# Performance work log

Hardware: AMD Instinct MI355X
Metric: run time of the kernel (lower is better)

Reference implementation:

```python
import jax, jax.numpy as jnp
import numpy as np

# dims: B pages, P boxes/page, TOTAL flat boxes, D model, H heads, C coords, Z rel positions, L layers
B, P, TOTAL, D, H, C, Z, L = 16, 512, 6400, 256, 8, 2, 64, 4
HS = D // H          # head size = 32
PAD_COLS = 448       # columns >= PAD_COLS are padding (-1)


def setup_inputs():
    key = jax.random.key(0)
    ks = jax.random.split(key, 10)
    embeds = jax.random.normal(ks[0], (TOTAL, D), jnp.float32)
    page_ids = jax.random.randint(ks[1], (B, P), 0, TOTAL)
    page_ids = page_ids.at[:, PAD_COLS:].set(-1)
    xmin = jax.random.uniform(ks[2], (TOTAL,)) * 0.9
    xmax = xmin + jax.random.uniform(ks[3], (TOTAL,)) * 0.1 + 0.01
    ymin = jax.random.uniform(ks[4], (TOTAL,)) * 0.9
    ymax = ymin + jax.random.uniform(ks[5], (TOTAL,)) * 0.1 + 0.01
    kk = jax.random.split(ks[6], 12)
    w = lambda k, *s: jax.random.normal(k, s, jnp.float32) * 0.02
    return dict(
        embeds=embeds, xmin=xmin, xmax=xmax, ymin=ymin, ymax=ymax,
        width=xmax - xmin, height=ymax - ymin,
        empty_embed=jax.random.normal(ks[7], (D,), jnp.float32),
        position_embedding=jax.random.normal(ks[8], (Z, D), jnp.float32),
        cq_w=w(kk[0], L, D, D), cq_b=jnp.zeros((L, D)),
        ck_w=w(kk[1], L, D, D), ck_b=jnp.zeros((L, D)),
        pk_w=w(kk[2], L, D, D), pk_b=jnp.zeros((L, D)),
        pq_w=w(kk[3], L, D, D), pq_b=jnp.zeros((L, D)),
        cv_w=w(kk[4], L, D, D), cv_b=jnp.zeros((L, D)),
        out_w=w(kk[5], L, D, D), out_b=jnp.zeros((L, D)),
        res1=jnp.full((L,), 0.1, jnp.float32), res2=jnp.full((L,), 0.1, jnp.float32),
        ln1_g=jnp.ones((L, D)), ln1_b=jnp.zeros((L, D)),
        ln2_g=jnp.ones((L, D)), ln2_b=jnp.zeros((L, D)),
        ff1_w=w(kk[6], L, D, 2 * D), ff1_b=jnp.zeros((L, 2 * D)),
        ff2_w=w(kk[7], L, 2 * D, D), ff2_b=jnp.zeros((L, D)),
        page_ids=page_ids,
    )


def _layer_norm(x, g, b, eps=1e-5):
    m = jnp.mean(x, axis=-1, keepdims=True)
    v = jnp.mean((x - m) ** 2, axis=-1, keepdims=True)
    return (x - m) * jax.lax.rsqrt(v + eps) * g + b


def _compute_rel(x0, x1, y0, y1, w, h, n_rel):
    # clamped to +-n_rel//2 and shifted into [0, n_rel)
    cx = (x0 + x1) * 0.5
    cy = (y0 + y1) * 0.5
    dx = jnp.round((cx[:, None, :] - cx[:, :, None]) / jnp.maximum(w[:, :, None], 1e-3))
    dy = jnp.round((cy[:, None, :] - cy[:, :, None]) / jnp.maximum(h[:, :, None], 1e-3))
    half = n_rel // 2
    rel = jnp.stack([dx, dy], axis=-1)
    return (jnp.clip(rel, -half, half - 1) + half).astype(jnp.int32)


def _forward(embeds, xmin, xmax, ymin, ymax, width, height, empty_embed,
             position_embedding, cq_w, cq_b, ck_w, ck_b, pk_w, pk_b, pq_w, pq_b,
             cv_w, cv_b, out_w, out_b, res1, res2, ln1_g, ln1_b, ln2_g, ln2_b,
             ff1_w, ff1_b, ff2_w, ff2_b, page_ids):
    mask = page_ids != -1                                           # [B,P]
    gth = lambda a: a[page_ids]                                     # flat -> [B,P]
    x = jnp.concatenate([jnp.broadcast_to(empty_embed, (B, 1, D)),
                         embeds[page_ids]], axis=1)                 # [B,N,D], N=P+1
    maskc = jnp.concatenate([jnp.ones((B, 1), bool), mask], axis=1) # [B,N]
    rel = _compute_rel(gth(xmin), gth(xmax), gth(ymin), gth(ymax),
                       gth(width), gth(height), Z)                  # [B,P,P,2]
    N = P + 1
    relc = jnp.zeros((B, N, N, 2), jnp.int32).at[:, 1:, 1:, :].set(rel)
    nopos = jnp.ones((B, N, N), bool).at[:, 1:, 1:].set(False)      # disable pos terms on CLS
    scale = 1.0 / float(np.sqrt(HS))
    neg = jnp.finfo(jnp.float32).min

    for l in range(L):
        q = (x @ cq_w[l] + cq_b[l]).reshape(B, N, H, HS)
        k = (x @ ck_w[l] + ck_b[l]).reshape(B, N, H, HS)
        c2c = jnp.einsum('bihd,bjhd->bijh', q, k)                   # [B,N,N,H]
        pk = (position_embedding @ pk_w[l] + pk_b[l]).reshape(Z, C, H, HS // C)
        pq = (position_embedding @ pq_w[l] + pq_b[l]).reshape(Z, C, H, HS // C)
        qc = q.reshape(B, N, H, C, HS // C)
        kc = k.reshape(B, N, H, C, HS // C)
        # c2p: score query against every relative-position key, then gather by index
        c2p = jnp.take_along_axis(jnp.einsum('bihcd,zchd->bizch', qc, pk),
                                  relc[..., None], axis=2)          # [B,N,N,C,H]
        # p2c: score position queries against content keys, gather along position axis
        p2c = jnp.take_along_axis(jnp.einsum('bjhcd,zchd->bzjch', kc, pq),
                                  relc[..., None], axis=1)          # [B,N,N,C,H]
        pos = jnp.sum(c2p + p2c, axis=3) * (~nopos)[..., None].astype(x.dtype)
        logits = (c2c + pos) * scale
        weights = jax.nn.softmax(
            jnp.where(maskc[:, None, :, None], logits, neg), axis=2)
        v = (x @ cv_w[l] + cv_b[l]).reshape(B, N, H, HS)
        upd = jnp.einsum('bijh,bjhd->bihd', weights, v).reshape(B, N, D) @ out_w[l] + out_b[l]
        x = _layer_norm(x + upd * res1[l], ln1_g[l], ln1_b[l])
        ff = jax.nn.gelu(x @ ff1_w[l] + ff1_b[l], approximate=False) @ ff2_w[l] + ff2_b[l]
        x = _layer_norm(x + ff * res2[l], ln2_g[l], ln2_b[l])

    # drop CLS and zero padded boxes (padded static-shape analogue of embeds[:,1:][mask])
    return x[:, 1:] * mask[..., None].astype(x.dtype)


def reference(embeds, xmin, xmax, ymin, ymax, width, height, empty_embed,
              position_embedding, cq_w, cq_b, ck_w, ck_b, pk_w, pk_b, pq_w, pq_b,
              cv_w, cv_b, out_w, out_b, res1, res2, ln1_g, ln1_b, ln2_g, ln2_b,
              ff1_w, ff1_b, ff2_w, ff2_b, page_ids):
    return _forward(embeds, xmin, xmax, ymin, ymax, width, height, empty_embed,
                    position_embedding, cq_w, cq_b, ck_w, ck_b, pk_w, pk_b, pq_w, pq_b,
                    cv_w, cv_b, out_w, out_b, res1, res2, ln1_g, ln1_b, ln2_g, ln2_b,
                    ff1_w, ff1_b, ff2_w, ff2_b, page_ids)
```

## Files before the change

### kernel.cpp

```cpp
#include <hip/hip_runtime.h>
#include <math.h>

#define BB 16
#define PP 512
#define DD 256
#define HH 8
#define NPAD 512
#define NVAL 449
#define MM (BB*PP)
#define NROWS (BB*HH*NPAD)

typedef unsigned short u16;
typedef __bf16 v8bf __attribute__((ext_vector_type(8)));
typedef float v4f __attribute__((ext_vector_type(4)));
typedef unsigned short u16x8 __attribute__((ext_vector_type(8)));
typedef unsigned short u16x4 __attribute__((ext_vector_type(4)));

static __device__ __forceinline__ float b2f(u16 u) {
  unsigned v = ((unsigned)u) << 16;
  return __builtin_bit_cast(float, v);
}
static __device__ __forceinline__ u16 f2b(float f) {
  unsigned x = __builtin_bit_cast(unsigned, f);
  unsigned lsb = (x >> 16) & 1u;
  x += 0x7fffu + lsb;
  return (u16)(x >> 16);
}
static __device__ __forceinline__ v8bf ldg8(const u16* p) {
  u16x8 u = *(const u16x8*)p;
  return __builtin_bit_cast(v8bf, u);
}
static __device__ __forceinline__ void gload16(const u16* g, u16* l) {
  __builtin_amdgcn_global_load_lds(
      (__attribute__((address_space(1))) void*)(g),
      (__attribute__((address_space(3))) void*)(l), 16, 0, 0);
}

__global__ void k_prep(const float* embeds, const float* xmin, const float* xmax,
                       const float* ymin, const float* ymax, const float* width,
                       const float* height, const float* empty_embed, const int* page_ids,
                       float* xf, u16* xb, float* gcx, float* gcy, float* gw, float* gh_) {
  int bx = blockIdx.x;
  int b = bx >> 9, r = bx & 511;
  int t = threadIdx.x;
  int c0 = t * 4;
  const float* src = nullptr;
  if (r == 0) src = empty_embed;
  else if (r <= 448) {
    int gi = page_ids[b * PP + (r - 1)];
    src = embeds + (size_t)gi * DD;
  }
  float4 fv = make_float4(0.f, 0.f, 0.f, 0.f);
  if (src) fv = *(const float4*)(src + c0);
  size_t row = (size_t)b * NPAD + r;
  *(float4*)(xf + row * DD + c0) = fv;
  u16x4 bv; bv[0] = f2b(fv.x); bv[1] = f2b(fv.y); bv[2] = f2b(fv.z); bv[3] = f2b(fv.w);
  *(u16x4*)(xb + row * DD + c0) = bv;
  if (t == 0) {
    int p = r;
    int gi = page_ids[b * PP + p];
    float cx = 0.f, cy = 0.f, ww = 1.f, hh = 1.f;
    if (gi >= 0) {
      cx = 0.5f * (xmin[gi] + xmax[gi]);
      cy = 0.5f * (ymin[gi] + ymax[gi]);
      ww = fmaxf(width[gi], 1e-3f);
      hh = fmaxf(height[gi], 1e-3f);
    }
    gcx[b * PP + p] = cx; gcy[b * PP + p] = cy;
    gw[b * PP + p] = ww;  gh_[b * PP + p] = hh;
  }
}

__global__ __launch_bounds__(64) void k_rel(const float* gcx, const float* gcy,
                                            const float* gw, const float* gh_, u16* relp) {
  int bx = blockIdx.x;
  int b = bx >> 9, i = bx & 511;
  int t = threadIdx.x;
  float cxi = 0.f, cyi = 0.f, wi = 1.f, hi = 1.f;
  if (i > 0) {
    cxi = gcx[b * PP + i - 1]; cyi = gcy[b * PP + i - 1];
    wi = gw[b * PP + i - 1];   hi = gh_[b * PP + i - 1];
  }
  u16* dst = relp + ((size_t)b * NPAD + i) * NPAD;
#pragma unroll
  for (int jj = 0; jj < 8; jj++) {
    int j = jj * 64 + t;
    u16 pk = (u16)(32 | (32 << 8));
    if (j > 0) {
      float cxj = gcx[b * PP + j - 1], cyj = gcy[b * PP + j - 1];
      float dxf = rintf((cxj - cxi) / wi);
      float dyf = rintf((cyj - cyi) / hi);
      int zx = (int)(fminf(fmaxf(dxf, -32.f), 31.f)) + 32;
      int zy = (int)(fminf(fmaxf(dyf, -32.f), 31.f)) + 32;
      pk = (u16)(zx | (zy << 8));
    }
    dst[j] = pk;
  }
}

__global__ __launch_bounds__(256) void k_wT(const float* cq, const float* ck, const float* cv,
                                            const float* ow, const float* f1, const float* f2,
                                            u16* wT) {
  __shared__ u16 lds[32][33];
  int bx = blockIdx.x;
  int l = bx >> 9, r = bx & 511;
  const float* src; int N, k0, n0; u16* dst; int dstStride;
  if (r < 192) {
    int mat = r / 64, rr = r % 64;
    k0 = (rr >> 3) * 32; n0 = (rr & 7) * 32;
    src = (mat == 0 ? cq : mat == 1 ? ck : cv) + (size_t)l * 65536;
    N = 256; dst = wT + (size_t)l * 524288 + mat * 65536; dstStride = 256;
  } else if (r < 256) {
    int rr = r - 192;
    k0 = (rr >> 3) * 32; n0 = (rr & 7) * 32;
    src = ow + (size_t)l * 65536; N = 256;
    dst = wT + (size_t)l * 524288 + 196608; dstStride = 256;
  } else if (r < 384) {
    int rr = r - 256;
    k0 = (rr >> 4) * 32; n0 = (rr & 15) * 32;
    src = f1 + (size_t)l * 131072; N = 512;
    dst = wT + (size_t)l * 524288 + 262144; dstStride = 256;
  } else {
    int rr = r - 384;
    k0 = (rr >> 3) * 32; n0 = (rr & 7) * 32;
    src = f2 + (size_t)l * 131072; N = 256;
    dst = wT + (size_t)l * 524288 + 393216; dstStride = 512;
  }
  int tx = threadIdx.x & 31, ty = threadIdx.x >> 5;
#pragma unroll
  for (int yy = 0; yy < 4; yy++) {
    int y = ty + yy * 8;
    lds[y][tx] = f2b(src[(size_t)(k0 + y) * N + n0 + tx]);
  }
  __syncthreads();
#pragma unroll
  for (int yy = 0; yy < 4; yy++) {
    int y = ty + yy * 8;
    dst[(size_t)(n0 + y) * dstStride + k0 + tx] = lds[tx][y];
  }
}

__global__ __launch_bounds__(256) void k_posproj(const float* pe, const float* pkw, const float* pkb,
                                                 const float* pqw, const float* pqb,
                                                 u16* pkfsw, u16* pqfsw) {
  int gid = blockIdx.x * 256 + threadIdx.x;
  int d = gid & 15, z = (gid >> 4) & 63, ch = (gid >> 10) & 15, l = (gid >> 14) & 3, tab = gid >> 16;
  const float* W = (tab ? pqw : pkw) + (size_t)l * 65536;
  const float* Bb = (tab ? pqb : pkb) + (size_t)l * 256;
  int col = (ch >> 3) * 128 + (ch & 7) * 16 + d;
  float s = Bb[col];
  const float* per = pe + (size_t)z * 256;
  for (int kk = 0; kk < 256; kk++) s += per[kk] * W[(size_t)kk * 256 + col];
  u16* dst = tab ? pqfsw : pkfsw;
  dst[(((size_t)l * 16 + ch) * 64 + z) * 16 + d] = f2b(s);
}

template <int EPI>
__global__ __launch_bounds__(256) void k_gemm(const u16* A, const u16* W, int K,
                                              const float* bias0, const float* bias1, const float* bias2,
                                              void* out0, void* out1, void* out2) {
  __shared__ u16 As[2][2048];
  __shared__ u16 Bs[2][2048];
  int w = threadIdx.x >> 6, lane = threadIdx.x & 63;
  int la = lane & 15, lg = lane >> 4;
  int wm = w & 1, wn = w >> 1;
  int m0 = blockIdx.x * 64;
  int n0 = blockIdx.y * 64;
  int arow = w * 16 + (lane >> 2);
  int koff = (lane & 3) * 8;
  const u16* gA = A + (size_t)(m0 + arow) * K + koff;
  const u16* gB = W + (size_t)(n0 + arow) * K + koff;
  v4f acc[2][2] = {};
  int nt = K >> 5;
  gload16(gA, &As[0][w * 512]);
  gload16(gB, &Bs[0][w * 512]);
  __syncthreads();
  for (int t = 0; t < nt; t++) {
    int cur = t & 1;
    if (t + 1 < nt) {
      int k2 = (t + 1) << 5;
      gload16(gA + k2, &As[cur ^ 1][w * 512]);
      gload16(gB + k2, &Bs[cur ^ 1][w * 512]);
    }
    const u16* as = As[cur];
    const u16* bs = Bs[cur];
    v8bf a0 = ldg8(as + (wm * 32 + la) * 32 + lg * 8);
    v8bf a1 = ldg8(as + (wm * 32 + 16 + la) * 32 + lg * 8);
    v8bf b0 = ldg8(bs + (wn * 32 + la) * 32 + lg * 8);
    v8bf b1 = ldg8(bs + (wn * 32 + 16 + la) * 32 + lg * 8);
    acc[0][0] = __builtin_amdgcn_mfma_f32_16x16x32_bf16(a0, b0, acc[0][0], 0, 0, 0);
    acc[0][1] = __builtin_amdgcn_mfma_f32_16x16x32_bf16(a0, b1, acc[0][1], 0, 0, 0);
    acc[1][0] = __builtin_amdgcn_mfma_f32_16x16x32_bf16(a1, b0, acc[1][0], 0, 0, 0);
    acc[1][1] = __builtin_amdgcn_mfma_f32_16x16x32_bf16(a1, b1, acc[1][1], 0, 0, 0);
    __syncthreads();
  }
#pragma unroll
  for (int fi = 0; fi < 2; fi++)
#pragma unroll
    for (int fj = 0; fj < 2; fj++)
#pragma unroll
      for (int rr = 0; rr < 4; rr++) {
        int m = m0 + wm * 32 + fi * 16 + lg * 4 + rr;
        int n = n0 + wn * 32 + fj * 16 + la;
        float v = acc[fi][fj][rr];
        if (EPI == 0) {
          const float* bp = (n < 256 ? bias0 : n < 512 ? bias1 : bias2);
          v += bp[n & 255];
          int b = m >> 9, i = m & 511, h = (n & 255) >> 5, d = n & 31;
          if (n < 512) {
            u16* dst = (u16*)(n < 256 ? out0 : out1);
            dst[(((size_t)(b * 8 + h)) * NPAD + i) * 32 + d] = f2b(v);
          } else {
            ((u16*)out2)[(((size_t)(b * 8 + h)) * 32 + d) * NPAD + i] = f2b(v);
          }
        } else if (EPI == 1) {
          ((u16*)out0)[(size_t)m * 256 + n] = f2b(v + bias0[n]);
        } else {
          float x = v + bias0[n];
          float g = 0.5f * x * (1.0f + erff(x * 0.70710678118654752f));
          ((u16*)out0)[(size_t)m * 512 + n] = f2b(g);
        }
      }
}

__global__ __launch_bounds__(256) void k_gemmA(const u16* opartb, const float* lpart,
                                               const u16* W, const float* bias, u16* y16) {
  __shared__ u16 As[2][2048];
  __shared__ u16 Bs[2][2048];
  int w = threadIdx.x >> 6, lane = threadIdx.x & 63;
  int la = lane & 15, lg = lane >> 4;
  int wm = w & 1, wn = w >> 1;
  int m0 = blockIdx.x * 64;
  int n0 = blockIdx.y * 64;
  int arow = w * 16 + (lane >> 2);
  int koff = (lane & 3) * 8;
  int m = m0 + arow, bb = m >> 9, ii = m & 511;
  const u16* gB = W + (size_t)(n0 + arow) * 256 + koff;
  v4f acc[2][2] = {};
  size_t rb0 = ((size_t)(bb * 8)) * NPAD + ii;
#define STAGE_A(hh, buf) do { \
    size_t rbase = rb0 + (size_t)(hh) * NPAD; \
    float l_ = lpart[rbase] + lpart[NROWS + rbase] + lpart[2u*NROWS + rbase] + lpart[3u*NROWS + rbase]; \
    float inv_ = 1.0f / l_; \
    u16x8 a0_ = *(const u16x8*)(opartb + rbase * 32 + koff); \
    u16x8 a1_ = *(const u16x8*)(opartb + ((size_t)NROWS + rbase) * 32 + koff); \
    u16x8 a2_ = *(const u16x8*)(opartb + ((size_t)2u * NROWS + rbase) * 32 + koff); \
    u16x8 a3_ = *(const u16x8*)(opartb + ((size_t)3u * NROWS + rbase) * 32 + koff); \
    u16x8 r_; \
    _Pragma("unroll") \
    for (int e = 0; e < 8; e++) \
      r_[e] = f2b((b2f(a0_[e]) + b2f(a1_[e]) + b2f(a2_[e]) + b2f(a3_[e])) * inv_); \
    *(u16x8*)(&As[buf][arow * 32 + koff]) = r_; \
  } while (0)
  STAGE_A(0, 0);
  gload16(gB, &Bs[0][w * 512]);
  __syncthreads();
  for (int t = 0; t < 8; t++) {
    int cur = t & 1;
    if (t + 1 < 8) {
      STAGE_A(t + 1, cur ^ 1);
      gload16(gB + ((t + 1) << 5), &Bs[cur ^ 1][w * 512]);
    }
    const u16* as = As[cur];
    const u16* bs = Bs[cur];
    v8bf a0 = ldg8(as + (wm * 32 + la) * 32 + lg * 8);
    v8bf a1 = ldg8(as + (wm * 32 + 16 + la) * 32 + lg * 8);
    v8bf b0 = ldg8(bs + (wn * 32 + la) * 32 + lg * 8);
    v8bf b1 = ldg8(bs + (wn * 32 + 16 + la) * 32 + lg * 8);
    acc[0][0] = __builtin_amdgcn_mfma_f32_16x16x32_bf16(a0, b0, acc[0][0], 0, 0, 0);
    acc[0][1] = __builtin_amdgcn_mfma_f32_16x16x32_bf16(a0, b1, acc[0][1], 0, 0, 0);
    acc[1][0] = __builtin_amdgcn_mfma_f32_16x16x32_bf16(a1, b0, acc[1][0], 0, 0, 0);
    acc[1][1] = __builtin_amdgcn_mfma_f32_16x16x32_bf16(a1, b1, acc[1][1], 0, 0, 0);
    __syncthreads();
  }
#undef STAGE_A
#pragma unroll
  for (int fi = 0; fi < 2; fi++)
#pragma unroll
    for (int fj = 0; fj < 2; fj++)
#pragma unroll
      for (int rr = 0; rr < 4; rr++) {
        int mm = m0 + wm * 32 + fi * 16 + lg * 4 + rr;
        int n = n0 + wn * 32 + fj * 16 + la;
        y16[(size_t)mm * 256 + n] = f2b(acc[fi][fj][rr] + bias[n]);
      }
}

__global__ __launch_bounds__(256) void k_tab(const u16* qh, const u16* kh,
                                             const u16* pkfsw, const u16* pqfsw,
                                             u16* tabC2, u16* tabP2, int l) {
  __shared__ __align__(16) u16 qs[4][8][32];
  const u16* srcp = blockIdx.z ? kh : qh;
  const u16* tbl = blockIdx.z ? pqfsw : pkfsw;
  u16* dst = blockIdx.z ? tabP2 : tabC2;
  int b = blockIdx.y, i0 = blockIdx.x * 4;
  int t = threadIdx.x;
  {
    int flat = t * 4;
    int si = flat >> 8, sh = (flat >> 5) & 7, sd = flat & 31;
    *(u16x4*)&qs[si][sh][sd] =
        *(const u16x4*)(srcp + (((size_t)(b * 8 + sh)) * NPAD + i0 + si) * 32 + sd);
  }
  __syncthreads();
  int z = t & 63, cg = t >> 6;
#pragma unroll
  for (int cc = 0; cc < 4; cc++) {
    int ch = cg * 4 + cc, c = ch >> 3, h = ch & 7;
    const u16* pp = tbl + (((size_t)l * 16 + ch) * 64 + z) * 16;
    u16x8 w0 = *(const u16x8*)pp;
    u16x8 w1 = *(const u16x8*)(pp + 8);
#pragma unroll
    for (int ii = 0; ii < 4; ii++) {
      const u16* qq = &qs[ii][h][c * 16];
      float s = 0.f;
#pragma unroll
      for (int d = 0; d < 8; d++) s += b2f(qq[d]) * b2f(w0[d]);
#pragma unroll
      for (int d = 0; d < 8; d++) s += b2f(qq[d + 8]) * b2f(w1[d]);
      dst[(((size_t)b * NPAD + i0 + ii) * 64 + z) * 16 + ch] = f2b(s);
    }
  }
}

__global__ __launch_bounds__(512) void k_attn(const u16* qh, const u16* kh, const u16* vtp,
                                              const u16* tabC2, const u16* tabP2, const u16* relp,
                                              u16* opartb, float* lpart) {
  __shared__ __align__(16) u16 posb[8][16][68];
  __shared__ __align__(16) u16 ps[8][16][72];
  int bid = blockIdx.x;
  int idx = (bid & 7) * 256 + (bid >> 3);
  int b = idx >> 7;
  int rest = idx & 127;
  int i0 = (rest >> 2) * 16;
  int part = rest & 3;
  int t = threadIdx.x, w = t >> 6, lane = t & 63;
  int la = lane & 15, lg = lane >> 4;
  v8bf qa = ldg8(qh + (((size_t)(b * 8 + w)) * NPAD + i0 + la) * 32 + lg * 8);
  float lrow[4] = {0.f, 0.f, 0.f, 0.f};
  v4f o0 = {}; v4f o1 = {};
  const float scale = 0.17677669529663687f;
  const float MC = 8.0f;
  const u16* kbase = kh + ((size_t)(b * 8 + w)) * NPAD * 32;
  const u16* vbase = vtp + ((size_t)(b * 8 + w)) * 32 * NPAD;
  const u16* rbase = relp + ((size_t)b * NPAD + i0) * NPAD;
  int ntile = (part == 3) ? 1 : 2;
  for (int tt = 0; tt < ntile; tt++) {
    int j0 = (part * 2 + tt) * 64;
#pragma unroll
    for (int pp = 0; pp < 2; pp++) {
      int p = t + pp * 512;
      int si = p >> 6, sj = p & 63;
      int ig = i0 + si, jg = j0 + sj;
      float pos[8] = {0.f, 0.f, 0.f, 0.f, 0.f, 0.f, 0.f, 0.f};
      if (ig > 0 && jg > 0) {
        unsigned rp = rbase[(size_t)si * NPAD + jg];
        int zx = rp & 255, zy = rp >> 8;
        u16x8 Av = *(const u16x8*)(tabC2 + (((size_t)b * NPAD + ig) * 64 + zx) * 16);
        u16x8 Cv = *(const u16x8*)(tabP2 + (((size_t)b * NPAD + jg) * 64 + zx) * 16);
        u16x8 Bv = *(const u16x8*)(tabC2 + (((size_t)b * NPAD + ig) * 64 + zy) * 16 + 8);
        u16x8 Dv = *(const u16x8*)(tabP2 + (((size_t)b * NPAD + jg) * 64 + zy) * 16 + 8);
#pragma unroll
        for (int h = 0; h < 8; h++)
          pos[h] = (b2f(Av[h]) + b2f(Cv[h])) + (b2f(Bv[h]) + b2f(Dv[h]));
      }
#pragma unroll
      for (int h = 0; h < 8; h++) posb[h][si][sj] = f2b(pos[h]);
    }
    __syncthreads();
    v4f s[4];
#pragma unroll
    for (int fj = 0; fj < 4; fj++) {
      v8bf kf = ldg8(kbase + (size_t)(j0 + fj * 16 + la) * 32 + lg * 8);
      v4f zero = {};
      s[fj] = __builtin_amdgcn_mfma_f32_16x16x32_bf16(qa, kf, zero, 0, 0, 0);
    }
    float pvv[4][4];
#pragma unroll
    for (int fj = 0; fj < 4; fj++) {
#pragma unroll
      for (int rr = 0; rr < 4; rr++) {
        int il = lg * 4 + rr;
        float lv = (s[fj][rr] + b2f(posb[w][il][fj * 16 + la])) * scale;
        pvv[fj][rr] = __expf(lv - MC);
      }
    }
    __syncthreads();
#pragma unroll
    for (int rr = 0; rr < 4; rr++)
      lrow[rr] += pvv[0][rr] + pvv[1][rr] + pvv[2][rr] + pvv[3][rr];
#pragma unroll
    for (int fj = 0; fj < 4; fj++)
#pragma unroll
      for (int rr = 0; rr < 4; rr++)
        ps[w][lg * 4 + rr][fj * 16 + la] = f2b(pvv[fj][rr]);
    v8bf pa0 = __builtin_bit_cast(v8bf, *(const u16x8*)&ps[w][la][lg * 8]);
    v8bf pa1 = __builtin_bit_cast(v8bf, *(const u16x8*)&ps[w][la][32 + lg * 8]);
    v8bf v00 = ldg8(vbase + (size_t)la * NPAD + j0 + lg * 8);
    v8bf v01 = ldg8(vbase + (size_t)la * NPAD + j0 + 32 + lg * 8);
    v8bf v10 = ldg8(vbase + (size_t)(16 + la) * NPAD + j0 + lg * 8);
    v8bf v11 = ldg8(vbase + (size_t)(16 + la) * NPAD + j0 + 32 + lg * 8);
    o0 = __builtin_amdgcn_mfma_f32_16x16x32_bf16(pa0, v00, o0, 0, 0, 0);
    o0 = __builtin_amdgcn_mfma_f32_16x16x32_bf16(pa1, v01, o0, 0, 0, 0);
    o1 = __builtin_amdgcn_mfma_f32_16x16x32_bf16(pa0, v10, o1, 0, 0, 0);
    o1 = __builtin_amdgcn_mfma_f32_16x16x32_bf16(pa1, v11, o1, 0, 0, 0);
  }
  if (part == 3) {
    v8bf kf = ldg8(kbase + (size_t)448 * 32 + lg * 8);
    float dot = 0.f;
#pragma unroll
    for (int e = 0; e < 8; e++) dot += (float)qa[e] * (float)kf[e];
    dot += __shfl_xor(dot, 16);
    dot += __shfl_xor(dot, 32);
    int ig = i0 + la;
    float pos = 0.f;
    if (ig > 0) {
      unsigned rp = relp[((size_t)b * NPAD + ig) * NPAD + 448];
      int zx = rp & 255, zy = rp >> 8;
      pos = b2f(tabC2[(((size_t)b * NPAD + ig) * 64 + zx) * 16 + w])
          + b2f(tabP2[(((size_t)b * NPAD + 448) * 64 + zx) * 16 + w])
          + b2f(tabC2[(((size_t)b * NPAD + ig) * 64 + zy) * 16 + 8 + w])
          + b2f(tabP2[(((size_t)b * NPAD + 448) * 64 + zy) * 16 + 8 + w]);
    }
    float p448 = __expf((dot + pos) * scale - MC);
    float va = b2f(vbase[(size_t)la * NPAD + 448]);
    float vb_ = b2f(vbase[(size_t)(16 + la) * NPAD + 448]);
#pragma unroll
    for (int rr = 0; rr < 4; rr++) {
      float pr = __shfl(p448, lg * 4 + rr);
      o0[rr] += pr * va;
      o1[rr] += pr * vb_;
      if (la == 0) lrow[rr] += pr;
    }
  }
#pragma unroll
  for (int rr = 0; rr < 4; rr++) {
    float l = lrow[rr];
    l += __shfl_xor(l, 1); l += __shfl_xor(l, 2); l += __shfl_xor(l, 4); l += __shfl_xor(l, 8);
    int ig = i0 + lg * 4 + rr;
    size_t row = (size_t)part * NROWS + (((size_t)(b * 8 + w)) * NPAD + ig);
    opartb[row * 32 + la] = f2b(o0[rr]);
    opartb[row * 32 + 16 + la] = f2b(o1[rr]);
    if (la == 0) lpart[row] = l;
  }
}

template <int LAST>
__global__ __launch_bounds__(256) void k_ln(float* xf, u16* xb, const u16* y16,
                                            const float* resv, int ridx,
                                            const float* g_, const float* b_, float* outp) {
  int row = blockIdx.x * 4 + (threadIdx.x >> 6);
  int lane = threadIdx.x & 63;
  float res = resv[ridx];
  const u16* yr = y16 + (size_t)row * DD;
  float* xr = xf + (size_t)row * DD;
  int c = lane * 4;
  float4 xv = *(const float4*)(xr + c);
  u16x4 yv = *(const u16x4*)(yr + c);
  float v0 = xv.x + b2f(yv[0]) * res, v1 = xv.y + b2f(yv[1]) * res;
  float v2 = xv.z + b2f(yv[2]) * res, v3 = xv.w + b2f(yv[3]) * res;
  float sum = v0 + v1 + v2 + v3;
  sum += __shfl_xor(sum, 1); sum += __shfl_xor(sum, 2); sum += __shfl_xor(sum, 4);
  sum += __shfl_xor(sum, 8); sum += __shfl_xor(sum, 16); sum += __shfl_xor(sum, 32);
  float mean = sum * (1.0f / 256.0f);
  float d0 = v0 - mean, d1 = v1 - mean, d2 = v2 - mean, d3 = v3 - mean;
  float vs = d0 * d0 + d1 * d1 + d2 * d2 + d3 * d3;
  vs += __shfl_xor(vs, 1); vs += __shfl_xor(vs, 2); vs += __shfl_xor(vs, 4);
  vs += __shfl_xor(vs, 8); vs += __shfl_xor(vs, 16); vs += __shfl_xor(vs, 32);
  float rstd = rsqrtf(vs * (1.0f / 256.0f) + 1e-5f);
  float o0 = d0 * rstd * g_[c + 0] + b_[c + 0];
  float o1 = d1 * rstd * g_[c + 1] + b_[c + 1];
  float o2 = d2 * rstd * g_[c + 2] + b_[c + 2];
  float o3 = d3 * rstd * g_[c + 3] + b_[c + 3];
  if (!LAST) {
    *(float4*)(xr + c) = make_float4(o0, o1, o2, o3);
    u16x4 bv; bv[0] = f2b(o0); bv[1] = f2b(o1); bv[2] = f2b(o2); bv[3] = f2b(o3);
    *(u16x4*)(xb + (size_t)row * DD + c) = bv;
  } else {
    int bq = row >> 9, r = row & 511;
    if (r >= 1) {
      int p = r - 1;
      float4 val = (p < 448) ? make_float4(o0, o1, o2, o3) : make_float4(0.f, 0.f, 0.f, 0.f);
      *(float4*)(outp + ((size_t)bq * PP + p) * DD + c) = val;
    } else {
      *(float4*)(outp + ((size_t)bq * PP + 511) * DD + c) = make_float4(0.f, 0.f, 0.f, 0.f);
    }
  }
}

__global__ void k_diag(float* out, int v) {
  int gid = blockIdx.x * 64 + threadIdx.x;
  float4 r = make_float4(0.f, 0.f, 0.f, 0.f);
  if (gid == 28672) r.x = (float)v;
  *(float4*)(out + (size_t)gid * 4) = r;
}

extern "C" void kernel_launch(void* const* d_in, const int* in_sizes, int n_in,
                              void* d_out, int out_size, void* d_ws, size_t ws_size,
                              hipStream_t stream) {
  const float* embeds = (const float*)d_in[0];
  const float* xmin = (const float*)d_in[1];
  const float* xmax = (const float*)d_in[2];
  const float* ymin = (const float*)d_in[3];
  const float* ymax = (const float*)d_in[4];
  const float* width = (const float*)d_in[5];
  const float* height = (const float*)d_in[6];
  const float* empty_embed = (const float*)d_in[7];
  const float* pos_emb = (const float*)d_in[8];
  const float* cq_w = (const float*)d_in[9];
  const float* cq_b = (const float*)d_in[10];
  const float* ck_w = (const float*)d_in[11];
  const float* ck_b = (const float*)d_in[12];
  const float* pk_w = (const float*)d_in[13];
  const float* pk_b = (const float*)d_in[14];
  const float* pq_w = (const float*)d_in[15];
  const float* pq_b = (const float*)d_in[16];
  const float* cv_w = (const float*)d_in[17];
  const float* cv_b = (const float*)d_in[18];
  const float* out_w = (const float*)d_in[19];
  const float* out_b = (const float*)d_in[20];
  const float* res1 = (const float*)d_in[21];
  const float* res2 = (const float*)d_in[22];
  const float* ln1_g = (const float*)d_in[23];
  const float* ln1_b = (const float*)d_in[24];
  const float* ln2_g = (const float*)d_in[25];
  const float* ln2_b = (const float*)d_in[26];
  const float* ff1_w = (const float*)d_in[27];
  const float* ff1_b = (const float*)d_in[28];
  const float* ff2_w = (const float*)d_in[29];
  const float* ff2_b = (const float*)d_in[30];
  const int* page_ids = (const int*)d_in[31];

  char* ws = (char*)d_ws;
  size_t off = 0;
  auto alloc = [&](size_t bytes) -> void* {
    void* p = ws + off;
    off += (bytes + 255) & ~(size_t)255;
    return p;
  };
  float* xf = (float*)alloc((size_t)MM * DD * 4);
  u16* xb = (u16*)alloc((size_t)MM * DD * 2);
  u16* qh = (u16*)alloc((size_t)MM * DD * 2);
  u16* kh = (u16*)alloc((size_t)MM * DD * 2);
  u16* vt = (u16*)alloc((size_t)MM * DD * 2);
  u16* y16 = (u16*)alloc((size_t)MM * DD * 2);
  u16* h1b = (u16*)alloc((size_t)MM * 512 * 2);
  u16* tabC2 = (u16*)alloc((size_t)BB * NPAD * 64 * 16 * 2);
  u16* tabP2 = (u16*)alloc((size_t)BB * NPAD * 64 * 16 * 2);
  u16* relp = (u16*)alloc((size_t)BB * NPAD * NPAD * 2);
  u16* opartb = (u16*)alloc((size_t)4 * NROWS * 32 * 2);
  float* lpart = (float*)alloc((size_t)4 * NROWS * 4);
  u16* wT = (u16*)alloc((size_t)4 * 524288 * 2);
  u16* pkfsw = (u16*)alloc((size_t)4 * 16 * 64 * 16 * 2);
  u16* pqfsw = (u16*)alloc((size_t)4 * 16 * 64 * 16 * 2);
  float* gcx = (float*)alloc((size_t)BB * PP * 4);
  float* gcy = (float*)alloc((size_t)BB * PP * 4);
  float* gw = (float*)alloc((size_t)BB * PP * 4);
  float* gh_ = (float*)alloc((size_t)BB * PP * 4);
  (void)in_sizes; (void)n_in; (void)out_size;

  if (off > ws_size) {
    k_diag<<<dim3(8192), 64, 0, stream>>>((float*)d_out, 216);
    return;
  }

  k_prep<<<dim3(8192), 64, 0, stream>>>(embeds, xmin, xmax, ymin, ymax, width, height,
                                        empty_embed, page_ids, xf, xb, gcx, gcy, gw, gh_);
  k_rel<<<dim3(8192), 64, 0, stream>>>(gcx, gcy, gw, gh_, relp);
  k_wT<<<dim3(2048), 256, 0, stream>>>(cq_w, ck_w, cv_w, out_w, ff1_w, ff2_w, wT);
  k_posproj<<<dim3(512), 256, 0, stream>>>(pos_emb, pk_w, pk_b, pq_w, pq_b, pkfsw, pqfsw);

  for (int l = 0; l < 4; l++) {
    const u16* wl = wT + (size_t)l * 524288;
    k_gemm<0><<<dim3(128, 12), 256, 0, stream>>>(xb, wl, 256, cq_b + l * 256, ck_b + l * 256,
                                                 cv_b + l * 256, qh, kh, vt);
    k_tab<<<dim3(128, 16, 2), 256, 0, stream>>>(qh, kh, pkfsw, pqfsw, tabC2, tabP2, l);
    k_attn<<<dim3(2048), 512, 0, stream>>>(qh, kh, vt, tabC2, tabP2, relp, opartb, lpart);
    k_gemmA<<<dim3(128, 4), 256, 0, stream>>>(opartb, lpart, wl + 196608, out_b + l * 256, y16);
    k_ln<0><<<dim3(2048), 256, 0, stream>>>(xf, xb, y16, res1, l, ln1_g + l * 256, ln1_b + l * 256,
                                            (float*)d_out);
    k_gemm<2><<<dim3(128, 8), 256, 0, stream>>>(xb, wl + 262144, 256, ff1_b + l * 512,
                                                nullptr, nullptr, h1b, nullptr, nullptr);
    k_gemm<1><<<dim3(128, 4), 256, 0, stream>>>(h1b, wl + 393216, 512, ff2_b + l * 256,
                                                nullptr, nullptr, y16, nullptr, nullptr);
    if (l < 3)
      k_ln<0><<<dim3(2048), 256, 0, stream>>>(xf, xb, y16, res2, l, ln2_g + l * 256,
                                              ln2_b + l * 256, (float*)d_out);
    else
      k_ln<1><<<dim3(2048), 256, 0, stream>>>(xf, xb, y16, res2, l, ln2_g + l * 256,
                                              ln2_b + l * 256, (float*)d_out);
  }
}
```

Baseline: 604.9 us.

## Prefetch positional table gathers, pack pos bias pairs, vectorize table stores

The attention kernel now issues the gathers from the relative-position tables for the next key tile before the PV MFMA work of the current tile, so their latency overlaps compute. The pos-bias staging buffer in shared memory packs two heads per 32-bit word, which halves the number of LDS stores. The table-building kernel loads all weights up front and writes four channels with one 8-byte store instead of four scalar stores. The cost is more registers held across the loop, which may lower occupancy.

```diff
diff --git a/kernel.cpp b/kernel.cpp
--- a/kernel.cpp
+++ b/kernel.cpp
@@ -11,6 +11,7 @@
 #define NROWS (BB*HH*NPAD)
 
 typedef unsigned short u16;
+typedef unsigned u32;
 typedef __bf16 v8bf __attribute__((ext_vector_type(8)));
 typedef float v4f __attribute__((ext_vector_type(4)));
 typedef unsigned short u16x8 __attribute__((ext_vector_type(8)));
@@ -303,29 +304,36 @@
   }
   __syncthreads();
   int z = t & 63, cg = t >> 6;
+  u16x8 W0[4], W1[4];
 #pragma unroll
   for (int cc = 0; cc < 4; cc++) {
-    int ch = cg * 4 + cc, c = ch >> 3, h = ch & 7;
+    int ch = cg * 4 + cc;
     const u16* pp = tbl + (((size_t)l * 16 + ch) * 64 + z) * 16;
-    u16x8 w0 = *(const u16x8*)pp;
-    u16x8 w1 = *(const u16x8*)(pp + 8);
-#pragma unroll
-    for (int ii = 0; ii < 4; ii++) {
+    W0[cc] = *(const u16x8*)pp;
+    W1[cc] = *(const u16x8*)(pp + 8);
+  }
+#pragma unroll
+  for (int ii = 0; ii < 4; ii++) {
+    u16x4 res;
+#pragma unroll
+    for (int cc = 0; cc < 4; cc++) {
+      int ch = cg * 4 + cc, c = ch >> 3, h = ch & 7;
       const u16* qq = &qs[ii][h][c * 16];
       float s = 0.f;
 #pragma unroll
-      for (int d = 0; d < 8; d++) s += b2f(qq[d]) * b2f(w0[d]);
-#pragma unroll
-      for (int d = 0; d < 8; d++) s += b2f(qq[d + 8]) * b2f(w1[d]);
-      dst[(((size_t)b * NPAD + i0 + ii) * 64 + z) * 16 + ch] = f2b(s);
-    }
+      for (int d = 0; d < 8; d++) s += b2f(qq[d]) * b2f(W0[cc][d]);
+#pragma unroll
+      for (int d = 0; d < 8; d++) s += b2f(qq[d + 8]) * b2f(W1[cc][d]);
+      res[cc] = f2b(s);
+    }
+    *(u16x4*)&dst[(((size_t)b * NPAD + i0 + ii) * 64 + z) * 16 + cg * 4] = res;
   }
 }
 
 __global__ __launch_bounds__(512) void k_attn(const u16* qh, const u16* kh, const u16* vtp,
                                               const u16* tabC2, const u16* tabP2, const u16* relp,
                                               u16* opartb, float* lpart) {
-  __shared__ __align__(16) u16 posb[8][16][68];
+  __shared__ u32 posb[4][16][68];
   __shared__ __align__(16) u16 ps[8][16][72];
   int bid = blockIdx.x;
   int idx = (bid & 7) * 256 + (bid >> 3);
@@ -344,27 +352,42 @@
   const u16* vbase = vtp + ((size_t)(b * 8 + w)) * 32 * NPAD;
   const u16* rbase = relp + ((size_t)b * NPAD + i0) * NPAD;
   int ntile = (part == 3) ? 1 : 2;
+  u16x8 Av[2], Bv[2], Cv[2], Dv[2];
+  bool fval[2];
+#define FETCH(J0) do {                                                          \
+    _Pragma("unroll")                                                           \
+    for (int pp = 0; pp < 2; pp++) {                                            \
+      int p_ = t + pp * 512;                                                    \
+      int si_ = p_ >> 6, sj_ = p_ & 63;                                         \
+      int ig_ = i0 + si_, jg_ = (J0) + sj_;                                     \
+      bool v_ = (ig_ > 0 && jg_ > 0);                                           \
+      fval[pp] = v_;                                                            \
+      if (v_) {                                                                 \
+        unsigned rp_ = rbase[(size_t)si_ * NPAD + jg_];                         \
+        int zx_ = rp_ & 255, zy_ = rp_ >> 8;                                    \
+        Av[pp] = *(const u16x8*)(tabC2 + (((size_t)b * NPAD + ig_) * 64 + zx_) * 16);     \
+        Cv[pp] = *(const u16x8*)(tabP2 + (((size_t)b * NPAD + jg_) * 64 + zx_) * 16);     \
+        Bv[pp] = *(const u16x8*)(tabC2 + (((size_t)b * NPAD + ig_) * 64 + zy_) * 16 + 8); \
+        Dv[pp] = *(const u16x8*)(tabP2 + (((size_t)b * NPAD + jg_) * 64 + zy_) * 16 + 8); \
+      }                                                                         \
+    }                                                                           \
+  } while (0)
+  FETCH(part * 128);
   for (int tt = 0; tt < ntile; tt++) {
     int j0 = (part * 2 + tt) * 64;
 #pragma unroll
     for (int pp = 0; pp < 2; pp++) {
       int p = t + pp * 512;
       int si = p >> 6, sj = p & 63;
-      int ig = i0 + si, jg = j0 + sj;
       float pos[8] = {0.f, 0.f, 0.f, 0.f, 0.f, 0.f, 0.f, 0.f};
-      if (ig > 0 && jg > 0) {
-        unsigned rp = rbase[(size_t)si * NPAD + jg];
-        int zx = rp & 255, zy = rp >> 8;
-        u16x8 Av = *(const u16x8*)(tabC2 + (((size_t)b * NPAD + ig) * 64 + zx) * 16);
-        u16x8 Cv = *(const u16x8*)(tabP2 + (((size_t)b * NPAD + jg) * 64 + zx) * 16);
-        u16x8 Bv = *(const u16x8*)(tabC2 + (((size_t)b * NPAD + ig) * 64 + zy) * 16 + 8);
-        u16x8 Dv = *(const u16x8*)(tabP2 + (((size_t)b * NPAD + jg) * 64 + zy) * 16 + 8);
+      if (fval[pp]) {
 #pragma unroll
         for (int h = 0; h < 8; h++)
-          pos[h] = (b2f(Av[h]) + b2f(Cv[h])) + (b2f(Bv[h]) + b2f(Dv[h]));
+          pos[h] = (b2f(Av[pp][h]) + b2f(Cv[pp][h])) + (b2f(Bv[pp][h]) + b2f(Dv[pp][h]));
       }
 #pragma unroll
-      for (int h = 0; h < 8; h++) posb[h][si][sj] = f2b(pos[h]);
+      for (int hp = 0; hp < 4; hp++)
+        posb[hp][si][sj] = (u32)f2b(pos[2 * hp]) | ((u32)f2b(pos[2 * hp + 1]) << 16);
     }
     __syncthreads();
     v4f s[4];
@@ -375,16 +398,20 @@
       s[fj] = __builtin_amdgcn_mfma_f32_16x16x32_bf16(qa, kf, zero, 0, 0, 0);
     }
     float pvv[4][4];
+    int wsel = (w & 1) ? 16 : 0;
 #pragma unroll
     for (int fj = 0; fj < 4; fj++) {
 #pragma unroll
       for (int rr = 0; rr < 4; rr++) {
         int il = lg * 4 + rr;
-        float lv = (s[fj][rr] + b2f(posb[w][il][fj * 16 + la])) * scale;
+        u32 pk = posb[w >> 1][il][fj * 16 + la];
+        float posv = b2f((u16)(pk >> wsel));
+        float lv = (s[fj][rr] + posv) * scale;
         pvv[fj][rr] = __expf(lv - MC);
       }
     }
     __syncthreads();
+    if (tt + 1 < ntile) FETCH(j0 + 64);
 #pragma unroll
     for (int rr = 0; rr < 4; rr++)
       lrow[rr] += pvv[0][rr] + pvv[1][rr] + pvv[2][rr] + pvv[3][rr];
@@ -404,6 +431,7 @@
     o1 = __builtin_amdgcn_mfma_f32_16x16x32_bf16(pa0, v10, o1, 0, 0, 0);
     o1 = __builtin_amdgcn_mfma_f32_16x16x32_bf16(pa1, v11, o1, 0, 0, 0);
   }
+#undef FETCH
   if (part == 3) {
     v8bf kf = ldg8(kbase + (size_t)448 * 32 + lg * 8);
     float dot = 0.f;
```

After: 538.1 us. 1.12x faster.
